# Optimization experiments

Hardware: AMD Instinct MI355X
Metric: run time of the kernel (lower is better)

Reference implementation:

```python
import jax, jax.numpy as jnp
import numpy as np

SPATIAL_SHAPES = np.array([[100, 100], [50, 50], [25, 25], [13, 13]], dtype=np.int32)
EMBED, NH, NL, NP = 256, 8, 4, 4
HD = EMBED // NH  # 32


def setup_inputs() -> dict:
    key = jax.random.key(0)
    ks = jax.random.split(key, 12)
    bs, nq = 4, 4000
    nv = int((SPATIAL_SHAPES[:, 0] * SPATIAL_SHAPES[:, 1]).sum())  # 13294
    s_lin = 1.0 / np.sqrt(EMBED)  # xavier-ish scale
    s_small = 0.02                # offsets/weights heads start near init
    return {
        "query": jax.random.normal(ks[0], (bs, nq, EMBED), jnp.float32),
        "value": jax.random.normal(ks[1], (bs, nv, EMBED), jnp.float32),
        "reference_points": jax.random.uniform(ks[2], (bs, nq, NL, 2), jnp.float32),
        "spatial_shapes": jnp.asarray(SPATIAL_SHAPES),
        "W_off": jax.random.normal(ks[3], (EMBED, NH * NL * NP * 2), jnp.float32) * s_small,
        "b_off": jax.random.normal(ks[4], (NH * NL * NP * 2,), jnp.float32) * s_small,
        "W_attn": jax.random.normal(ks[5], (EMBED, NH * NL * NP), jnp.float32) * s_small,
        "b_attn": jax.random.normal(ks[6], (NH * NL * NP,), jnp.float32) * s_small,
        "W_val": jax.random.normal(ks[7], (EMBED, EMBED), jnp.float32) * s_lin,
        "b_val": jnp.zeros((EMBED,), jnp.float32),
        "W_out": jax.random.normal(ks[8], (EMBED, EMBED), jnp.float32) * s_lin,
        "b_out": jnp.zeros((EMBED,), jnp.float32),
    }


def _bilinear_sample(val_l, H, W, x, y):
    """grid_sample(mode=bilinear, padding=zeros, align_corners=False) equivalent.
    val_l: [bs, nh, H*W, hd]; x, y: [bs, nh, nq, np] pixel-space coords.
    Returns [bs, nh, nq, np, hd]."""
    x0 = jnp.floor(x)
    y0 = jnp.floor(y)
    bs, nh, nq, npts = x.shape
    out = 0.0
    for dx, dy in ((0, 0), (1, 0), (0, 1), (1, 1)):
        xi = x0 + dx
        yi = y0 + dy
        w = (1.0 - jnp.abs(x - xi)) * (1.0 - jnp.abs(y - yi))
        valid = (xi >= 0) & (xi < W) & (yi >= 0) & (yi < H)
        idx = (jnp.clip(yi, 0, H - 1) * W + jnp.clip(xi, 0, W - 1)).astype(jnp.int32)
        g = jnp.take_along_axis(val_l, idx.reshape(bs, nh, nq * npts, 1), axis=2)
        g = g.reshape(bs, nh, nq, npts, -1)
        out = out + g * (w * valid.astype(w.dtype))[..., None]
    return out


def reference(query, value, reference_points, spatial_shapes,
              W_off, b_off, W_attn, b_attn, W_val, b_val, W_out, b_out):
    shapes = np.asarray(spatial_shapes)  # static level shapes
    bs, nq, _ = query.shape
    # value projection -> per-head layout [bs, nh, nv, hd]
    v = (value @ W_val + b_val).reshape(bs, -1, NH, HD).transpose(0, 2, 1, 3)
    # sampling offsets and attention weights from query
    off = (query @ W_off + b_off).reshape(bs, nq, NH, NL, NP, 2)
    attn = jax.nn.softmax((query @ W_attn + b_attn).reshape(bs, nq, NH, NL * NP), axis=-1)
    attn = attn.reshape(bs, nq, NH, NL, NP)
    # normalized sampling locations; normalizer = (W, H) per level
    normalizer = jnp.asarray(np.stack([shapes[:, 1], shapes[:, 0]], -1), jnp.float32)
    loc = reference_points[:, :, None, :, None, :] + off / normalizer[None, None, None, :, None, :]
    out = jnp.zeros((bs, NH, nq, HD), query.dtype)
    start = 0
    for l in range(NL):
        H, W = int(shapes[l, 0]), int(shapes[l, 1])
        val_l = v[:, :, start:start + H * W, :]
        # pixel coords with align_corners=False: p = loc*size - 0.5
        x = loc[:, :, :, l, :, 0].transpose(0, 2, 1, 3) * W - 0.5  # [bs,nh,nq,np]
        y = loc[:, :, :, l, :, 1].transpose(0, 2, 1, 3) * H - 0.5
        sampled = _bilinear_sample(val_l, H, W, x, y)  # [bs,nh,nq,np,hd]
        out = out + jnp.einsum('bhqpd,bqhp->bhqd', sampled, attn[:, :, :, l, :])
        start += H * W
    out = out.transpose(0, 2, 1, 3).reshape(bs, nq, EMBED)
    return out @ W_out + b_out
```

## Files before the change

### kernel.cpp

```cpp
#include <hip/hip_runtime.h>
#include <hip/hip_bf16.h>

#define EMBED 256
#define NH 8
#define NL 4
#define NP 4
#define HD 32
#define BS 4
#define NQ 4000
#define NV 13294

using f32x4   = __attribute__((ext_vector_type(4))) float;
using bf16x8  = __attribute__((ext_vector_type(8))) short;

__device__ __forceinline__ float bf2f_lo(unsigned u) {
    union { unsigned u; float f; } x; x.u = u << 16; return x.f;
}
__device__ __forceinline__ float bf2f_hi(unsigned u) {
    union { unsigned u; float f; } x; x.u = u & 0xffff0000u; return x.f;
}
__device__ __forceinline__ unsigned short f2bf(float f) {
    union { float f; unsigned u; } x; x.f = f;
    unsigned u = x.u;
    return (unsigned short)((u + 0x7fffu + ((u >> 16) & 1u)) >> 16);
}
__device__ __forceinline__ unsigned cvtpk(float lo, float hi) {
    unsigned r;
    asm("v_cvt_pk_bf16_f32 %0, %1, %2" : "=v"(r) : "v"(lo), "v"(hi));
    return r;
}

__device__ __forceinline__ void async16(const void* g, void* l) {
    __builtin_amdgcn_global_load_lds(
        (const __attribute__((address_space(1))) void*)g,
        (__attribute__((address_space(3))) void*)l, 16, 0, 0);
}

template<int N> __device__ __forceinline__ void wait_vmcnt() {
    if constexpr (N == 0)      asm volatile("s_waitcnt vmcnt(0)" ::: "memory");
    else if constexpr (N == 3) asm volatile("s_waitcnt vmcnt(3)" ::: "memory");
    else if constexpr (N == 4) asm volatile("s_waitcnt vmcnt(4)" ::: "memory");
}

__global__ __launch_bounds__(256) void msda_prep_k(
    const float* __restrict__ W_val, const float* __restrict__ W_out,
    const float* __restrict__ W_off, const float* __restrict__ W_attn,
    const float* __restrict__ b_off, const float* __restrict__ b_attn,
    unsigned short* __restrict__ Wt_val, unsigned short* __restrict__ Wt_out,
    unsigned short* __restrict__ Wt_qa, float* __restrict__ b_qa)
{
    int i = blockIdx.x * 256 + threadIdx.x;
    if (i < 384) b_qa[i] = (i < 256) ? b_off[i] : b_attn[i - 256];
    if (i < 65536) {
        int r = i >> 8, c = i & 255;
        Wt_val[c * 256 + r] = f2bf(W_val[i]);
    } else if (i < 131072) {
        int j = i - 65536, r = j >> 8, c = j & 255;
        Wt_out[c * 256 + r] = f2bf(W_out[j]);
    } else if (i < 229376) {
        int j = i - 131072;
        int n = j >> 8, k = j & 255;
        float v = (n < 256) ? W_off[k * 256 + n] : W_attn[k * 128 + (n - 256)];
        Wt_qa[j] = f2bf(v);
    }
}

template<int EPI, bool ABF16>
__device__ __forceinline__ void gemm_body(
    char* lds,
    const void* __restrict__ Ap,
    const unsigned short* __restrict__ Bt,
    const float* __restrict__ bias,
    void* __restrict__ out,
    int M, int N, int mblk, int nblk)
{
    constexpr int K = 256, C = 8;
    constexpr int NI = 2;
    constexpr int ABYTES = 64 * 32 * 2;
    constexpr int BBYTES = 128 * 32 * 2;
    constexpr int BUFB   = ABYTES + BBYTES;
    constexpr int LOPS   = ABF16 ? 1 : 2;

    const int m0 = mblk * 64, n0 = nblk * 128;
    const int tid  = threadIdx.x;
    const int w    = tid >> 6;
    const int lane = tid & 63;
    const int quad = lane >> 4;
    const int l16  = lane & 15;
    const int wn   = w * 32;

    const int ar  = w * 16 + (lane >> 2);
    const int arg = min(m0 + ar, M - 1);
    const int ak  = (lane & 3) * 8;
    const float*          afp = (const float*)Ap          + (size_t)arg * K + ak;
    const unsigned short* abp = (const unsigned short*)Ap + (size_t)arg * K + ak;

    const int brseg = lane >> 2, bcb = (lane & 3) * 16;
    const char* bgp0 = (const char*)(Bt + (size_t)(n0 + (2 * w) * 16 + brseg) * K) + bcb;
    const char* bgp1 = (const char*)(Bt + (size_t)(n0 + (2 * w + 1) * 16 + brseg) * K) + bcb;

    auto issueB = [&](int c, int kb) {
        char* bL = lds + kb * BUFB + ABYTES;
        async16(bgp0 + c * 64, bL + (2 * w) * 1024);
        async16(bgp1 + c * 64, bL + (2 * w + 1) * 1024);
    };

    float4 aLoR[2], aHiR[2];
    bf16x8 aRegR[2];
    auto loadA = [&](int c) {
        const int p = c & 1;
        if constexpr (ABF16) {
            aRegR[p] = *(const bf16x8*)(abp + c * 32);
        } else {
            aLoR[p] = *(const float4*)(afp + c * 32);
            aHiR[p] = *(const float4*)(afp + c * 32 + 4);
        }
    };
    auto writeA = [&](int c) {
        const int p = c & 1;
        unsigned short* dst = (unsigned short*)(lds + (c % 3) * BUFB) + ar * 32 + ak;
        if constexpr (ABF16) {
            *(bf16x8*)dst = aRegR[p];
        } else {
            union { unsigned u[4]; bf16x8 v; } t;
            t.u[0] = cvtpk(aLoR[p].x, aLoR[p].y); t.u[1] = cvtpk(aLoR[p].z, aLoR[p].w);
            t.u[2] = cvtpk(aHiR[p].x, aHiR[p].y); t.u[3] = cvtpk(aHiR[p].z, aHiR[p].w);
            *(bf16x8*)dst = t.v;
        }
    };

    f32x4 acc[4][NI];
#pragma unroll
    for (int a = 0; a < 4; a++)
#pragma unroll
        for (int b = 0; b < NI; b++) acc[a][b] = (f32x4){0.f, 0.f, 0.f, 0.f};

    loadA(0); issueB(0, 0); loadA(1); issueB(1, 1);
    writeA(0);

#pragma unroll
    for (int c = 0; c < C; c++) {
        if (c < C - 1) wait_vmcnt<LOPS + 2>(); else wait_vmcnt<0>();
        asm volatile("s_waitcnt lgkmcnt(0)" ::: "memory");
        __builtin_amdgcn_s_barrier();
        __builtin_amdgcn_sched_barrier(0);
        if (c + 2 < C) { loadA(c + 2); issueB(c + 2, (c + 2) % 3); }

        const char* aL = lds + (c % 3) * BUFB;
        const char* bL = aL + ABYTES;
        bf16x8 af[4], bfr[NI];
#pragma unroll
        for (int mi = 0; mi < 4; mi++)
            af[mi] = *(const bf16x8*)(aL + (mi * 16 + l16) * 64 + quad * 16);
#pragma unroll
        for (int ni = 0; ni < NI; ni++)
            bfr[ni] = *(const bf16x8*)(bL + (wn + ni * 16 + l16) * 64 + quad * 16);

        if (c + 1 < C) writeA(c + 1);

#pragma unroll
        for (int mi = 0; mi < 4; mi++)
#pragma unroll
            for (int ni = 0; ni < NI; ni++)
                acc[mi][ni] = __builtin_amdgcn_mfma_f32_16x16x32_bf16(af[mi], bfr[ni], acc[mi][ni], 0, 0, 0);
    }

    if constexpr (EPI == 0) {
        __syncthreads();
        unsigned short* cs = (unsigned short*)lds;
#pragma unroll
        for (int ni = 0; ni < NI; ni++) {
            int cl = wn + ni * 16 + l16;
            float bvv = bias[n0 + cl];
#pragma unroll
            for (int mi = 0; mi < 4; mi++)
#pragma unroll
                for (int r = 0; r < 4; r++) {
                    int ml = mi * 16 + quad * 4 + r;
                    cs[ml * 136 + cl] = f2bf(acc[mi][ni][r] + bvv);
                }
        }
        __syncthreads();
        const int rr = w * 16 + (lane >> 2);
        const int jj = lane & 3;
        const int m  = m0 + rr;
        if (m < M) {
            const int b   = m / NV;
            const int pix = m - b * NV;
#pragma unroll
            for (int seg = 0; seg < 4; seg++) {
                const int h = (n0 >> 5) + seg;
                uint4 s = *(const uint4*)&cs[rr * 136 + seg * 32 + jj * 8];
                *(uint4*)((char*)out + (((size_t)b * 8 + h) * NV + pix) * 64 + jj * 16) = s;
            }
        }
    } else {
#pragma unroll
        for (int ni = 0; ni < NI; ni++) {
            int cc = n0 + wn + ni * 16 + l16;
            float bvv = bias[cc];
#pragma unroll
            for (int mi = 0; mi < 4; mi++)
#pragma unroll
                for (int r = 0; r < 4; r++) {
                    int m = m0 + mi * 16 + quad * 4 + r;
                    if (m >= M) continue;
                    ((float*)out)[(size_t)m * N + cc] = acc[mi][ni][r] + bvv;
                }
        }
    }
}

__global__ __launch_bounds__(256) void msda_gemm_vq_k(
    const float* __restrict__ value, const float* __restrict__ query,
    const unsigned short* __restrict__ Wt_val, const unsigned short* __restrict__ Wt_qa,
    const float* __restrict__ b_val, const float* __restrict__ b_qa,
    unsigned short* __restrict__ v_buf, float* __restrict__ oa_buf)
{
    extern __shared__ char lds[];
    const int bx = blockIdx.x;
    if (bx < 1662) {
        gemm_body<0, false>(lds, value, Wt_val, b_val, v_buf,
                            BS * NV, 256, bx >> 1, bx & 1);
    } else {
        const int j = bx - 1662;
        const int mb = j / 3;
        gemm_body<1, false>(lds, query, Wt_qa, b_qa, oa_buf,
                            BS * NQ, 384, mb, j - mb * 3);
    }
}

__global__ __launch_bounds__(256) void msda_gemm_out_k(
    const unsigned short* __restrict__ t_buf,
    const unsigned short* __restrict__ Wt_out,
    const float* __restrict__ b_out,
    float* __restrict__ out)
{
    extern __shared__ char lds[];
    const int bx = blockIdx.x;
    gemm_body<1, true>(lds, t_buf, Wt_out, b_out, out,
                       BS * NQ, 256, bx >> 1, bx & 1);
}

__global__ __launch_bounds__(256) void msda_sampler_k(
    const float* __restrict__ refpts,
    const float* __restrict__ oa_buf,
    const unsigned short* __restrict__ v_buf,
    unsigned short* __restrict__ t_out)
{
    __shared__ float  oa_s[4][384];
    __shared__ float  ref_s[4][8];
    __shared__ float4 wtab[528];
    __shared__ int4   itab[528];

    const int tid = threadIdx.x;
    const int q0  = blockIdx.x * 4;

    {
        const float4* src = (const float4*)(oa_buf + (size_t)q0 * 384);
        float4* dst = (float4*)&oa_s[0][0];
        dst[tid] = src[tid];
        if (tid < 128) dst[256 + tid] = src[256 + tid];
        if (tid < 32) ((float*)ref_s)[tid] = refpts[q0 * 8 + tid];
    }
    __syncthreads();

    const int HWs[4]    = {100, 50, 25, 13};
    const int starts[4] = {0, 10000, 12500, 13125};
#pragma unroll
    for (int it = 0; it < 2; it++) {
        int s  = tid + it * 256;
        int i  = s & 15;
        int h  = (s >> 4) & 7;
        int ql = s >> 7;
        int l  = i >> 2, p = i & 3;
        float logit = oa_s[ql][256 + h * 16 + i];
        float m = logit;
#pragma unroll
        for (int off = 1; off < 16; off <<= 1) m = fmaxf(m, __shfl_xor(m, off, 64));
        float e = __expf(logit - m);
        float sum = e;
#pragma unroll
        for (int off = 1; off < 16; off <<= 1) sum += __shfl_xor(sum, off, 64);
        float a = e / sum;

        int Wl = HWs[l];
        float fW = (float)Wl;
        float rx = ref_s[ql][l * 2], ry = ref_s[ql][l * 2 + 1];
        float offx = oa_s[ql][h * 32 + l * 8 + p * 2];
        float offy = oa_s[ql][h * 32 + l * 8 + p * 2 + 1];
        float x = rx * fW + offx - 0.5f;
        float y = ry * fW + offy - 0.5f;
        float xf = floorf(x), yf = floorf(y);
        float fx = x - xf, fy = y - yf;
        int x0 = (int)xf, y0 = (int)yf;
        int x1 = x0 + 1, y1 = y0 + 1;
        float wx0 = (x0 >= 0 && x0 < Wl) ? (1.f - fx) : 0.f;
        float wx1 = (x1 >= 0 && x1 < Wl) ? fx : 0.f;
        float wy0 = (y0 >= 0 && y0 < Wl) ? (1.f - fy) : 0.f;
        float wy1 = (y1 >= 0 && y1 < Wl) ? fy : 0.f;
        int x0c = min(max(x0, 0), Wl - 1), x1c = min(max(x1, 0), Wl - 1);
        int y0c = min(max(y0, 0), Wl - 1), y1c = min(max(y1, 0), Wl - 1);
        int r0 = starts[l] + y0c * Wl, r1 = starts[l] + y1c * Wl;
        int ti = i * 33 + ql * 8 + h;
        wtab[ti] = make_float4(wx0 * wy0 * a, wx1 * wy0 * a, wx0 * wy1 * a, wx1 * wy1 * a);
        itab[ti] = make_int4(r0 + x0c, r0 + x1c, r1 + x0c, r1 + x1c);
    }
    __syncthreads();

    const int dg = tid & 7, h = (tid >> 3) & 7, ql = tid >> 6;
    const int q = q0 + ql;
    const int b = q / NQ;
    const char* base = (const char*)v_buf + ((size_t)(b * 8 + h)) * NV * 64 + dg * 8;
    const int tbase = ql * 8 + h;

    float a0 = 0.f, a1 = 0.f, a2 = 0.f, a3 = 0.f;
#pragma unroll
    for (int lp = 0; lp < 16; lp++) {
        float4 wv = wtab[lp * 33 + tbase];
        int4   ix = itab[lp * 33 + tbase];
        uint2 s0 = *(const uint2*)(base + ((unsigned)ix.x << 6));
        uint2 s1 = *(const uint2*)(base + ((unsigned)ix.y << 6));
        uint2 s2 = *(const uint2*)(base + ((unsigned)ix.z << 6));
        uint2 s3 = *(const uint2*)(base + ((unsigned)ix.w << 6));
        a0 += wv.x * bf2f_lo(s0.x); a1 += wv.x * bf2f_hi(s0.x);
        a2 += wv.x * bf2f_lo(s0.y); a3 += wv.x * bf2f_hi(s0.y);
        a0 += wv.y * bf2f_lo(s1.x); a1 += wv.y * bf2f_hi(s1.x);
        a2 += wv.y * bf2f_lo(s1.y); a3 += wv.y * bf2f_hi(s1.y);
        a0 += wv.z * bf2f_lo(s2.x); a1 += wv.z * bf2f_hi(s2.x);
        a2 += wv.z * bf2f_lo(s2.y); a3 += wv.z * bf2f_hi(s2.y);
        a0 += wv.w * bf2f_lo(s3.x); a1 += wv.w * bf2f_hi(s3.x);
        a2 += wv.w * bf2f_lo(s3.y); a3 += wv.w * bf2f_hi(s3.y);
    }
    unsigned o0 = (unsigned)f2bf(a0) | ((unsigned)f2bf(a1) << 16);
    unsigned o1 = (unsigned)f2bf(a2) | ((unsigned)f2bf(a3) << 16);
    uint2 o = {o0, o1};
    *(uint2*)(t_out + (size_t)q * 256 + h * 32 + dg * 4) = o;
}

extern "C" void kernel_launch(void* const* d_in, const int* in_sizes, int n_in,
                              void* d_out, int out_size, void* d_ws, size_t ws_size,
                              hipStream_t stream) {
    const float* query  = (const float*)d_in[0];
    const float* value  = (const float*)d_in[1];
    const float* refpts = (const float*)d_in[2];
    const float* W_off  = (const float*)d_in[4];
    const float* b_off  = (const float*)d_in[5];
    const float* W_attn = (const float*)d_in[6];
    const float* b_attn = (const float*)d_in[7];
    const float* W_val  = (const float*)d_in[8];
    const float* b_val  = (const float*)d_in[9];
    const float* W_out  = (const float*)d_in[10];
    const float* b_out  = (const float*)d_in[11];

    char* wsp = (char*)d_ws;
    size_t o = 0;
    auto carve = [&](size_t bytes) -> void* {
        void* p = wsp + o; o += (bytes + 255) & ~(size_t)255; return p;
    };
    unsigned short* Wt_val = (unsigned short*)carve(256 * 256 * 2);
    unsigned short* Wt_out = (unsigned short*)carve(256 * 256 * 2);
    unsigned short* Wt_qa  = (unsigned short*)carve(384 * 256 * 2);
    float*          b_qa   = (float*)carve(384 * 4);
    unsigned short* v_buf  = (unsigned short*)carve((size_t)BS * NH * NV * 32 * 2);
    float*          oa_buf = (float*)carve((size_t)BS * NQ * 384 * 4);
    unsigned short* t_buf  = (unsigned short*)carve((size_t)BS * NQ * EMBED * 2);

    msda_prep_k<<<896, 256, 0, stream>>>(W_val, W_out, W_off, W_attn,
                                         b_off, b_attn, Wt_val, Wt_out, Wt_qa, b_qa);

    msda_gemm_vq_k<<<1662 + 750, 256, 36864, stream>>>(value, query, Wt_val, Wt_qa,
                                                       b_val, b_qa, v_buf, oa_buf);
    msda_sampler_k<<<(BS * NQ) / 4, 256, 0, stream>>>(refpts, oa_buf, v_buf, t_buf);
    msda_gemm_out_k<<<500, 256, 36864, stream>>>(t_buf, Wt_out, b_out, (float*)d_out);
}
```

Before: 196.0 us.

## Enlarge GEMM tiles to 128x128 with 512-thread blocks and 8 waves

The shared GEMM body now uses 128x128 output tiles computed by eight waves in a 2x4 arrangement instead of 64x128 tiles with four waves. Each thread loads one A row segment and one B segment per k-chunk, and the vmcnt waits are adjusted to match. The aim is to halve the block count and raise operand reuse per LDS load, cutting global and LDS traffic per output. The cost is more LDS per block (48 KB) and fewer blocks, which may lower occupancy and tail balance, especially for the small output GEMM with only 250 blocks.

```diff
diff --git a/kernel.cpp b/kernel.cpp
--- a/kernel.cpp
+++ b/kernel.cpp
@@ -38,8 +38,8 @@
 
 template<int N> __device__ __forceinline__ void wait_vmcnt() {
     if constexpr (N == 0)      asm volatile("s_waitcnt vmcnt(0)" ::: "memory");
+    else if constexpr (N == 2) asm volatile("s_waitcnt vmcnt(2)" ::: "memory");
     else if constexpr (N == 3) asm volatile("s_waitcnt vmcnt(3)" ::: "memory");
-    else if constexpr (N == 4) asm volatile("s_waitcnt vmcnt(4)" ::: "memory");
 }
 
 __global__ __launch_bounds__(256) void msda_prep_k(
@@ -76,33 +76,30 @@
 {
     constexpr int K = 256, C = 8;
     constexpr int NI = 2;
-    constexpr int ABYTES = 64 * 32 * 2;
-    constexpr int BBYTES = 128 * 32 * 2;
-    constexpr int BUFB   = ABYTES + BBYTES;
+    constexpr int ABYTES = 128 * 32 * 2;
+    constexpr int BUFB   = ABYTES + 128 * 32 * 2;
     constexpr int LOPS   = ABF16 ? 1 : 2;
 
-    const int m0 = mblk * 64, n0 = nblk * 128;
+    const int m0 = mblk * 128, n0 = nblk * 128;
     const int tid  = threadIdx.x;
     const int w    = tid >> 6;
     const int lane = tid & 63;
     const int quad = lane >> 4;
     const int l16  = lane & 15;
-    const int wn   = w * 32;
-
-    const int ar  = w * 16 + (lane >> 2);
+    const int wm   = (w & 1) * 64;
+    const int wn   = (w >> 1) * 32;
+
+    const int ar  = tid >> 2;
     const int arg = min(m0 + ar, M - 1);
-    const int ak  = (lane & 3) * 8;
+    const int ak  = (tid & 3) * 8;
     const float*          afp = (const float*)Ap          + (size_t)arg * K + ak;
     const unsigned short* abp = (const unsigned short*)Ap + (size_t)arg * K + ak;
 
-    const int brseg = lane >> 2, bcb = (lane & 3) * 16;
-    const char* bgp0 = (const char*)(Bt + (size_t)(n0 + (2 * w) * 16 + brseg) * K) + bcb;
-    const char* bgp1 = (const char*)(Bt + (size_t)(n0 + (2 * w + 1) * 16 + brseg) * K) + bcb;
+    const char* bgp = (const char*)(Bt + (size_t)(n0 + w * 16 + (lane >> 2)) * K)
+                      + (lane & 3) * 16;
 
     auto issueB = [&](int c, int kb) {
-        char* bL = lds + kb * BUFB + ABYTES;
-        async16(bgp0 + c * 64, bL + (2 * w) * 1024);
-        async16(bgp1 + c * 64, bL + (2 * w + 1) * 1024);
+        async16(bgp + c * 64, lds + kb * BUFB + ABYTES + w * 1024);
     };
 
     float4 aLoR[2], aHiR[2];
@@ -140,7 +137,7 @@
 
 #pragma unroll
     for (int c = 0; c < C; c++) {
-        if (c < C - 1) wait_vmcnt<LOPS + 2>(); else wait_vmcnt<0>();
+        if (c < C - 1) wait_vmcnt<LOPS + 1>(); else wait_vmcnt<0>();
         asm volatile("s_waitcnt lgkmcnt(0)" ::: "memory");
         __builtin_amdgcn_s_barrier();
         __builtin_amdgcn_sched_barrier(0);
@@ -151,7 +148,7 @@
         bf16x8 af[4], bfr[NI];
 #pragma unroll
         for (int mi = 0; mi < 4; mi++)
-            af[mi] = *(const bf16x8*)(aL + (mi * 16 + l16) * 64 + quad * 16);
+            af[mi] = *(const bf16x8*)(aL + (wm + mi * 16 + l16) * 64 + quad * 16);
 #pragma unroll
         for (int ni = 0; ni < NI; ni++)
             bfr[ni] = *(const bf16x8*)(bL + (wn + ni * 16 + l16) * 64 + quad * 16);
@@ -176,23 +173,21 @@
             for (int mi = 0; mi < 4; mi++)
 #pragma unroll
                 for (int r = 0; r < 4; r++) {
-                    int ml = mi * 16 + quad * 4 + r;
+                    int ml = wm + mi * 16 + quad * 4 + r;
                     cs[ml * 136 + cl] = f2bf(acc[mi][ni][r] + bvv);
                 }
         }
         __syncthreads();
-        const int rr = w * 16 + (lane >> 2);
-        const int jj = lane & 3;
-        const int m  = m0 + rr;
+        const int seg = tid >> 7, rr = tid & 127;
+        const int m = m0 + rr;
         if (m < M) {
             const int b   = m / NV;
             const int pix = m - b * NV;
-#pragma unroll
-            for (int seg = 0; seg < 4; seg++) {
-                const int h = (n0 >> 5) + seg;
-                uint4 s = *(const uint4*)&cs[rr * 136 + seg * 32 + jj * 8];
-                *(uint4*)((char*)out + (((size_t)b * 8 + h) * NV + pix) * 64 + jj * 16) = s;
-            }
+            const int h   = (n0 >> 5) + seg;
+            char* dst = (char*)out + (((size_t)b * 8 + h) * NV + pix) * 64;
+            const uint4* s = (const uint4*)&cs[rr * 136 + seg * 32];
+#pragma unroll
+            for (int j = 0; j < 4; j++) ((uint4*)dst)[j] = s[j];
         }
     } else {
 #pragma unroll
@@ -203,7 +198,7 @@
             for (int mi = 0; mi < 4; mi++)
 #pragma unroll
                 for (int r = 0; r < 4; r++) {
-                    int m = m0 + mi * 16 + quad * 4 + r;
+                    int m = m0 + wm + mi * 16 + quad * 4 + r;
                     if (m >= M) continue;
                     ((float*)out)[(size_t)m * N + cc] = acc[mi][ni][r] + bvv;
                 }
@@ -211,7 +206,7 @@
     }
 }
 
-__global__ __launch_bounds__(256) void msda_gemm_vq_k(
+__global__ __launch_bounds__(512) void msda_gemm_vq_k(
     const float* __restrict__ value, const float* __restrict__ query,
     const unsigned short* __restrict__ Wt_val, const unsigned short* __restrict__ Wt_qa,
     const float* __restrict__ b_val, const float* __restrict__ b_qa,
@@ -219,18 +214,18 @@
 {
     extern __shared__ char lds[];
     const int bx = blockIdx.x;
-    if (bx < 1662) {
+    if (bx < 832) {
         gemm_body<0, false>(lds, value, Wt_val, b_val, v_buf,
                             BS * NV, 256, bx >> 1, bx & 1);
     } else {
-        const int j = bx - 1662;
+        const int j = bx - 832;
         const int mb = j / 3;
         gemm_body<1, false>(lds, query, Wt_qa, b_qa, oa_buf,
                             BS * NQ, 384, mb, j - mb * 3);
     }
 }
 
-__global__ __launch_bounds__(256) void msda_gemm_out_k(
+__global__ __launch_bounds__(512) void msda_gemm_out_k(
     const unsigned short* __restrict__ t_buf,
     const unsigned short* __restrict__ Wt_out,
     const float* __restrict__ b_out,
@@ -369,8 +364,8 @@
     msda_prep_k<<<896, 256, 0, stream>>>(W_val, W_out, W_off, W_attn,
                                          b_off, b_attn, Wt_val, Wt_out, Wt_qa, b_qa);
 
-    msda_gemm_vq_k<<<1662 + 750, 256, 36864, stream>>>(value, query, Wt_val, Wt_qa,
-                                                       b_val, b_qa, v_buf, oa_buf);
+    msda_gemm_vq_k<<<832 + 375, 512, 49152, stream>>>(value, query, Wt_val, Wt_qa,
+                                                      b_val, b_qa, v_buf, oa_buf);
     msda_sampler_k<<<(BS * NQ) / 4, 256, 0, stream>>>(refpts, oa_buf, v_buf, t_buf);
-    msda_gemm_out_k<<<500, 256, 36864, stream>>>(t_buf, Wt_out, b_out, (float*)d_out);
-}
+    msda_gemm_out_k<<<250, 512, 49152, stream>>>(t_buf, Wt_out, b_out, (float*)d_out);
+}
```

After: 196.0 us. Within noise of the previous version (+0.0%).
